# Optimization experiments

Hardware: AMD Instinct MI355X
Metric: run time of the kernel (lower is better)

## Reference

```python
import jax, jax.numpy as jnp
import numpy as np

N_NODES = 20000
N_EDGES = 240000
N_GRAPHS = 200
D_IN = 118
H = 256          # simplified hidden width standing in for the mul=50 irreps hidden
NB = 10          # number_of_basis
RH = 100         # fc_neurons hidden
L = 3            # layers
SH = 9           # lmax=2 -> 1+3+5 spherical-harmonic channels
MAX_RADIUS = 5.0
NUM_NEIGHBORS = 12.0


def setup_inputs() -> dict:
    key = jax.random.key(0)
    ks = jax.random.split(key, 16)
    inp = {
        "x": jax.random.normal(ks[0], (N_NODES, D_IN), jnp.float32),
        "pos": jax.random.normal(ks[1], (N_NODES, 3), jnp.float32),
        "edge_shift": jax.random.normal(ks[2], (N_EDGES, 3), jnp.float32),
        "lattice": jax.random.normal(ks[3], (N_GRAPHS, 3, 3), jnp.float32),
        "W_embed": jax.random.normal(ks[4], (D_IN, H), jnp.float32) / np.sqrt(D_IN),
        "r1": jax.random.normal(ks[5], (L, NB, RH), jnp.float32) / np.sqrt(NB),
        "b1": jax.random.normal(ks[6], (L, RH), jnp.float32) * 0.1,
        "r2": jax.random.normal(ks[7], (L, RH, H), jnp.float32) / np.sqrt(RH),
        "Wtp": jax.random.normal(ks[8], (L, SH, H, H), jnp.float32) / np.sqrt(SH * H),
        "Wself": jax.random.normal(ks[9], (L, H, H), jnp.float32) / np.sqrt(H),
        "Wskip": jax.random.normal(ks[10], (L, H, H), jnp.float32) / np.sqrt(H),
        "Wout": jax.random.normal(ks[11], (H, 1), jnp.float32) / np.sqrt(H),
        "edge_index": jax.random.randint(ks[12], (2, N_EDGES), 0, N_NODES, jnp.int64)
                        if jax.config.jax_enable_x64 else
                      jax.random.randint(ks[12], (2, N_EDGES), 0, N_NODES).astype(jnp.int32),
        "batch": jnp.sort(jax.random.randint(ks[13], (N_NODES,), 0, N_GRAPHS)).astype(jnp.int32),
    }
    return inp


def _sph_harm_lmax2(u):
    """Component-normalized real spherical harmonics up to l=2 on unit vectors u [E,3]."""
    x, y, z = u[:, 0], u[:, 1], u[:, 2]
    c1 = np.sqrt(3.0)
    c2 = np.sqrt(15.0)
    return jnp.stack([
        jnp.ones_like(x),                       # l=0
        c1 * x, c1 * y, c1 * z,                 # l=1
        c2 * x * y, c2 * y * z,                 # l=2
        (np.sqrt(5.0) / 2.0) * (3.0 * z * z - 1.0),
        c2 * x * z, (c2 / 2.0) * (x * x - y * y),
    ], axis=1)                                  # [E, 9]


def _soft_one_hot_cosine(lens):
    """e3nn soft_one_hot_linspace(basis='cosine', cutoff=True) * sqrt(NB)."""
    vals = jnp.linspace(0.0, MAX_RADIUS, NB + 2)
    step = vals[1] - vals[0]
    vals = vals[1:-1]
    diff = (lens[:, None] - vals[None, :]) / step          # [E, NB]
    emb = jnp.cos(0.5 * jnp.pi * diff) * (diff > -1.0) * (diff < 1.0)
    return emb * np.sqrt(float(NB))


def _forward(x, pos, edge_shift, lattice, W_embed, r1, b1, r2, Wtp, Wself, Wskip, Wout,
             edge_src, edge_dst, batch):
    edge_batch = batch[edge_src]                            # [E]
    # periodic edge vectors: pos[dst] - pos[src] + shift @ lattice[graph]
    edge_vec = pos[edge_dst] - pos[edge_src] + jnp.einsum(
        'ni,nij->nj', edge_shift, lattice[edge_batch])      # [E, 3]
    lens = jnp.linalg.norm(edge_vec, axis=1)                # [E]
    u = edge_vec / (lens[:, None] + 1e-12)
    sh = _sph_harm_lmax2(u)                                 # [E, 9]
    emb = _soft_one_hot_cosine(lens)                        # [E, NB]

    h = x @ W_embed                                         # [N, H]
    inv_sqrt_deg = 1.0 / np.sqrt(NUM_NEIGHBORS)
    for l in range(L):
        radial = jax.nn.silu(emb @ r1[l] + b1[l]) @ r2[l]   # [E, H]
        hs = h[edge_src] * radial                           # gather + radial gate
        # weighted tensor-product-like message: sum_a (hs * sh_a) @ Wtp[l, a]
        msg = (hs * sh[:, 0:1]) @ Wtp[l, 0]
        for a in range(1, SH):
            msg = msg + (hs * sh[:, a:a + 1]) @ Wtp[l, a]   # [E, H]
        agg = jax.ops.segment_sum(msg, edge_dst, num_segments=N_NODES) * inv_sqrt_deg
        h = jax.nn.gelu(agg @ Wself[l] + h @ Wskip[l])      # [N, H]

    node_out = h @ Wout                                     # [N, 1]
    # scatter_mean over graphs
    sums = jax.ops.segment_sum(node_out, batch, num_segments=N_GRAPHS)
    cnts = jax.ops.segment_sum(jnp.ones((N_NODES, 1), node_out.dtype), batch,
                               num_segments=N_GRAPHS)
    return sums / jnp.maximum(cnts, 1.0)                    # [G, 1]


def reference(x, pos, edge_shift, lattice, W_embed, r1, b1, r2, Wtp, Wself, Wskip, Wout,
              edge_index, batch):
    return _forward(x, pos, edge_shift, lattice, W_embed, r1, b1, r2, Wtp, Wself, Wskip,
                    Wout, edge_index[0], edge_index[1], batch)
```

## Files before the change

kernel.cpp:

```cpp
#include <hip/hip_runtime.h>
#include <hip/hip_bf16.h>
#include <cstddef>
#include <cstdint>

#define NNODE  20000
#define MPAD   20096
#define NEDGE  240000
#define NGRAPH 200
#define DIN    118
#define HD     256
#define NBASIS 10
#define RHID   100
#define NLAYER 3
#define NSH    9
#define SHSTR  16
#define KTP    (NSH * HD)
#define KTOT   (KTP + HD)
#define KR2    128
#define KEMB   128
#define NRT    (MPAD / 64)

typedef _Float16 f16;
typedef _Float16 f16x2 __attribute__((ext_vector_type(2)));
typedef _Float16 f16x4 __attribute__((ext_vector_type(4)));
typedef _Float16 f16x8 __attribute__((ext_vector_type(8)));
typedef float    f32x4 __attribute__((ext_vector_type(4)));

__device__ __forceinline__ float gelu_tanh(float v) {
  float v3 = v * v * v;
  return 0.5f * v * (1.f + tanhf(0.7978845608028654f * (v + 0.044715f * v3)));
}

__device__ __forceinline__ void gload16(const void* g, void* l) {
  __builtin_amdgcn_global_load_lds(
      (const __attribute__((address_space(1))) unsigned int*)g,
      (__attribute__((address_space(3))) unsigned int*)l, 16, 0, 0);
}

__device__ __forceinline__ int perm64(int rho) {
  return (rho & ~63) | ((rho & 15) * 4 + ((rho >> 4) & 3));
}
__device__ __forceinline__ int inv_perm64(int n) {
  return (n & ~63) | (((n & 3) << 4) | ((n >> 2) & 15));
}

__global__ void deg_hist_kernel(const int* __restrict__ ei, int* __restrict__ deg)
{
  int e = blockIdx.x * 256 + threadIdx.x;
  if (e >= NEDGE) return;
  atomicAdd(&deg[ei[NEDGE + e]], 1);
}

__global__ void scan_kernel(const int* __restrict__ deg, int* __restrict__ rowptr)
{
  __shared__ int part[256];
  int t = threadIdx.x;
  const int chunk = (NNODE + 255) / 256;
  int start = t * chunk;
  int end = min(start + chunk, NNODE);
  int s = 0;
  for (int i = start; i < end; ++i) s += deg[i];
  part[t] = s;
  __syncthreads();
  for (int off = 1; off < 256; off <<= 1) {
    int v = (t >= off) ? part[t - off] : 0;
    __syncthreads();
    part[t] += v;
    __syncthreads();
  }
  int run = (t == 0) ? 0 : part[t - 1];
  for (int i = start; i < end; ++i) { rowptr[i] = run; run += deg[i]; }
  if (t == 255) rowptr[NNODE] = run;
}

__global__ void edge_geom_kernel(const float* __restrict__ pos,
                                 const float* __restrict__ shift,
                                 const float* __restrict__ lat,
                                 const int* __restrict__ ei,
                                 const int* __restrict__ batch,
                                 const int* __restrict__ rowptr,
                                 int* __restrict__ cursor,
                                 f16* __restrict__ sh_s,
                                 float* __restrict__ lens_s)
{
  int e = blockIdx.x * 256 + threadIdx.x;
  if (e >= NEDGE) return;
  int src = ei[e];
  int dst = ei[NEDGE + e];
  int b = batch[src];
  const float* L = lat + (size_t)b * 9;
  float s0 = shift[e * 3 + 0], s1 = shift[e * 3 + 1], s2 = shift[e * 3 + 2];
  float ev[3];
#pragma unroll
  for (int j = 0; j < 3; ++j)
    ev[j] = pos[dst * 3 + j] - pos[src * 3 + j] + s0 * L[j] + s1 * L[3 + j] + s2 * L[6 + j];
  float len = sqrtf(ev[0] * ev[0] + ev[1] * ev[1] + ev[2] * ev[2]);
  float inv = 1.f / (len + 1e-12f);
  float x = ev[0] * inv, y = ev[1] * inv, z = ev[2] * inv;
  const float c1 = 1.7320508075688772f;
  const float c2 = 3.872983346207417f;
  int p = atomicAdd(&cursor[dst], 1);
  int si = rowptr[dst] + p;
  f16* she = sh_s + (size_t)si * SHSTR;
  she[0] = (f16)1.f;
  she[1] = (f16)(c1 * x);
  she[2] = (f16)(c1 * y);
  she[3] = (f16)(c1 * z);
  she[4] = (f16)(c2 * x * y);
  she[5] = (f16)(c2 * y * z);
  she[6] = (f16)(1.1180339887498949f * (3.f * z * z - 1.f));
  she[7] = (f16)(c2 * x * z);
  she[8] = (f16)(1.9364916731037085f * (x * x - y * y));
  she[9] = (f16)0.f;
  *(int*)(she + 10) = src;
  she[12] = (f16)0.f; she[13] = (f16)0.f; she[14] = (f16)0.f; she[15] = (f16)0.f;
  lens_s[si] = len;
}

__global__ void prep_kernel(const float* __restrict__ Wtp_l,
                            const float* __restrict__ Wself_l,
                            const float* __restrict__ Wskip_l,
                            const float* __restrict__ r2l,
                            const float* __restrict__ r1l,
                            const float* __restrict__ b1l,
                            f16* __restrict__ Wtp16,
                            f16* __restrict__ WselfT16,
                            f16* __restrict__ Bcat,
                            f16* __restrict__ r2h,
                            f16* __restrict__ r1h)
{
  int b = blockIdx.x, t = threadIdx.x;
  if (b < KTP) {
    int i = b * 256 + t;
    Wtp16[i] = (f16)Wtp_l[i];
  } else if (b < KTP + 256) {
    int n = b - KTP;
    WselfT16[(size_t)n * HD + t] = (f16)(Wself_l[(size_t)t * HD + n] * 0.28867513459481287f);
  } else if (b < KTP + 512) {
    int rho = b - KTP - 256;
    int pcol = perm64(rho);
    Bcat[(size_t)rho * KTOT + KTP + t] = (f16)Wskip_l[(size_t)t * HD + pcol];
  } else if (b < KTP + 768) {
    int rho = b - KTP - 512;
    if (t < KR2) {
      int p = perm64(rho);
      r2h[(size_t)rho * KR2 + t] = (t < RHID) ? (f16)r2l[(size_t)t * HD + p] : (f16)0.f;
    }
  } else {
#pragma unroll
    for (int u = 0; u < 16; ++u) {
      int idx = u * 256 + t;
      int n = idx >> 5, j = idx & 31;
      float v = 0.f;
      if (n < RHID) {
        if (j < NBASIS) v = r1l[(size_t)j * RHID + n];
        else if (j == NBASIS) v = b1l[n];
      }
      r1h[idx] = (f16)v;
    }
  }
}

__global__ void convert_x_kernel(const float* __restrict__ x, f16* __restrict__ xh)
{
  int i = blockIdx.x * 2 + (threadIdx.x >> 7);
  int k = threadIdx.x & 127;
  xh[(size_t)i * KEMB + k] = (i < NNODE && k < DIN) ? (f16)x[(size_t)i * DIN + k] : (f16)0.f;
}

__global__ void convert_wemb_kernel(const float* __restrict__ Wemb, f16* __restrict__ WembT16)
{
  int n = blockIdx.x, k = threadIdx.x;
  WembT16[(size_t)n * KEMB + k] = (k < DIN) ? (f16)Wemb[(size_t)k * HD + n] : (f16)0.f;
}

__global__ __launch_bounds__(256) void gemm_nt_kernel(
    const f16* __restrict__ A, const f16* __restrict__ B,
    f16* __restrict__ C, int K, int ldc, int permRows)
{
  __shared__ __align__(16) f16 As[4][64][8];
  __shared__ __align__(16) f16 Bs[4][128][8];
  int t = threadIdx.x;
  int lane = t & 63, w = t >> 6;
  int row0 = blockIdx.x * 64;
  int n0 = blockIdx.y * 128;
  f32x4 acc[2][4];
#pragma unroll
  for (int i = 0; i < 2; ++i)
#pragma unroll
    for (int j = 0; j < 4; ++j) acc[i][j] = (f32x4){0.f, 0.f, 0.f, 0.f};
  int mq = (w & 1) * 32, nq = (w >> 1) * 64;
  for (int k0 = 0; k0 < K; k0 += 32) {
    {
      int row = t & 63, cc = t >> 6;
      *(uint4*)&As[cc][row][0] = *(const uint4*)(A + (size_t)(row0 + row) * K + k0 + cc * 8);
    }
#pragma unroll
    for (int u = 0; u < 2; ++u) {
      int idx = t + u * 256;
      int ch = idx >> 7, nn = idx & 127;
      *(uint4*)&Bs[ch][nn][0] = *(const uint4*)(B + (size_t)(n0 + nn) * K + k0 + ch * 8);
    }
    __syncthreads();
    int q = lane >> 4, r = lane & 15;
    f16x8 af[2], bfr[4];
#pragma unroll
    for (int i = 0; i < 2; ++i) af[i] = *(const f16x8*)&As[q][mq + i * 16 + r][0];
#pragma unroll
    for (int j = 0; j < 4; ++j) bfr[j] = *(const f16x8*)&Bs[q][nq + j * 16 + r][0];
#pragma unroll
    for (int i = 0; i < 2; ++i)
#pragma unroll
      for (int j = 0; j < 4; ++j)
        acc[i][j] = __builtin_amdgcn_mfma_f32_16x16x32_f16(af[i], bfr[j], acc[i][j], 0, 0, 0);
    __syncthreads();
  }
  int q4 = ((lane >> 4)) * 4, cl = lane & 15;
#pragma unroll
  for (int i = 0; i < 2; ++i)
#pragma unroll
    for (int rr = 0; rr < 4; ++rr) {
      int row = row0 + mq + i * 16 + q4 + rr;
      int orow = permRows ? inv_perm64(row) : row;
#pragma unroll
      for (int j = 0; j < 4; ++j)
        C[(size_t)orow * ldc + n0 + nq + j * 16 + cl] = (f16)acc[i][j][rr];
    }
}

#define RHSTR 136
__global__ __launch_bounds__(256) void radial_kernel(
    const float* __restrict__ lens_s,
    const f16* __restrict__ r1h,
    const f16* __restrict__ r2h,
    f16* __restrict__ rad)
{
  __shared__ __align__(16) f16 emb_s[64][40];
  __shared__ __align__(16) f16 rhA[64 * RHSTR];
  int t = threadIdx.x;
  int lane = t & 63, w = t >> 6;
  int r = lane & 15, q = lane >> 4;
  int e0 = blockIdx.x * 64;

  {
    float len = lens_s[e0 + lane];
    const float step = 5.f / 11.f;
    const float sq = 3.1622776601683795f;
    f16x8 v;
#pragma unroll
    for (int kk = 0; kk < 8; ++kk) {
      int j = w * 8 + kk;
      float val = 0.f;
      if (j < NBASIS) {
        float d = (len - (float)(j + 1) * step) / step;
        val = (d > -1.f && d < 1.f) ? (__cosf(1.5707963267948966f * d) * sq) : 0.f;
      } else if (j == NBASIS) {
        val = 1.f;
      }
      v[kk] = (f16)val;
    }
    *(f16x8*)&emb_s[lane][w * 8] = v;
  }

  int n0w = w * 64;
  f16x8 bfr[4][4];
#pragma unroll
  for (int j = 0; j < 4; ++j)
#pragma unroll
    for (int ks = 0; ks < 4; ++ks)
      bfr[j][ks] = *(const f16x8*)(r2h + (size_t)(n0w + j * 16 + r) * KR2 + ks * 32 + q * 8);

  f16x8 b1f[2];
#pragma unroll
  for (int j = 0; j < 2; ++j)
    b1f[j] = *(const f16x8*)(r1h + (size_t)((2 * w + j) * 16 + r) * 32 + q * 8);

  __syncthreads();

  f32x4 acc1[4][2];
#pragma unroll
  for (int i = 0; i < 4; ++i)
#pragma unroll
    for (int j = 0; j < 2; ++j) acc1[i][j] = (f32x4){0.f, 0.f, 0.f, 0.f};
  {
    f16x8 a1f[4];
#pragma unroll
    for (int i = 0; i < 4; ++i)
      a1f[i] = *(const f16x8*)&emb_s[i * 16 + r][q * 8];
#pragma unroll
    for (int i = 0; i < 4; ++i)
#pragma unroll
      for (int j = 0; j < 2; ++j)
        acc1[i][j] = __builtin_amdgcn_mfma_f32_16x16x32_f16(a1f[i], b1f[j], acc1[i][j], 0, 0, 0);
  }

#pragma unroll
  for (int i = 0; i < 4; ++i)
#pragma unroll
    for (int j = 0; j < 2; ++j)
#pragma unroll
      for (int rr = 0; rr < 4; ++rr) {
        float s = acc1[i][j][rr];
        s = __fdividef(s, 1.f + __expf(-s));
        rhA[(i * 16 + q * 4 + rr) * RHSTR + (2 * w + j) * 16 + r] = (f16)s;
      }
  __syncthreads();

  f32x4 acc[4][4];
#pragma unroll
  for (int i = 0; i < 4; ++i)
#pragma unroll
    for (int j = 0; j < 4; ++j) acc[i][j] = (f32x4){0.f, 0.f, 0.f, 0.f};
#pragma unroll
  for (int ks = 0; ks < 4; ++ks) {
    f16x8 af[4];
#pragma unroll
    for (int i = 0; i < 4; ++i)
      af[i] = *(const f16x8*)&rhA[(i * 16 + r) * RHSTR + ks * 32 + q * 8];
#pragma unroll
    for (int i = 0; i < 4; ++i)
#pragma unroll
      for (int j = 0; j < 4; ++j)
        acc[i][j] = __builtin_amdgcn_mfma_f32_16x16x32_f16(af[i], bfr[j][ks], acc[i][j], 0, 0, 0);
  }

#pragma unroll
  for (int i = 0; i < 4; ++i)
#pragma unroll
    for (int rr = 0; rr < 4; ++rr) {
      int m = i * 16 + q * 4 + rr;
      f16x4 o;
#pragma unroll
      for (int j = 0; j < 4; ++j) o[j] = (f16)acc[i][j][rr];
      *(f16x4*)(rad + (size_t)(e0 + m) * HD + n0w + r * 4) = o;
    }
}

__global__ __launch_bounds__(256) void gather2_kernel(
    const int* __restrict__ rowptr, const f16* __restrict__ rad,
    const f16* __restrict__ h, const f16* __restrict__ sh_s,
    f16* __restrict__ T)
{
  int t = threadIdx.x;
  int half = t >> 7, lc = t & 127;
  int base = blockIdx.x * 4;
  for (int s = 0; s < 2; ++s) {
    int n = base + s * 2 + half;
    int beg = rowptr[n], end = rowptr[n + 1];
    float a0[NSH], a1[NSH];
#pragma unroll
    for (int a = 0; a < NSH; ++a) { a0[a] = 0.f; a1[a] = 0.f; }
    int j = beg;
    for (; j + 2 <= end; j += 2) {
      const f16* she0 = sh_s + (size_t)j * SHSTR;
      const f16* she1 = she0 + SHSTR;
      f16x8 s80 = *(const f16x8*)she0;
      f16x8 s81 = *(const f16x8*)she1;
      float s8v0 = (float)she0[8];
      float s8v1 = (float)she1[8];
      int src0 = *(const int*)(she0 + 10);
      int src1 = *(const int*)(she1 + 10);
      f16x2 rv0 = *(const f16x2*)(rad + (size_t)j * HD + 2 * lc);
      f16x2 rv1 = *(const f16x2*)(rad + (size_t)(j + 1) * HD + 2 * lc);
      f16x2 hv0 = *(const f16x2*)(h + (size_t)src0 * HD + 2 * lc);
      f16x2 hv1 = *(const f16x2*)(h + (size_t)src1 * HD + 2 * lc);
      float p00 = (float)rv0[0] * (float)hv0[0];
      float p01 = (float)rv0[1] * (float)hv0[1];
      float p10 = (float)rv1[0] * (float)hv1[0];
      float p11 = (float)rv1[1] * (float)hv1[1];
#pragma unroll
      for (int a = 0; a < 8; ++a) {
        float sv0 = (float)s80[a], sv1 = (float)s81[a];
        a0[a] += sv0 * p00 + sv1 * p10;
        a1[a] += sv0 * p01 + sv1 * p11;
      }
      a0[8] += s8v0 * p00 + s8v1 * p10;
      a1[8] += s8v0 * p01 + s8v1 * p11;
    }
    if (j < end) {
      const f16* she = sh_s + (size_t)j * SHSTR;
      f16x8 s8 = *(const f16x8*)she;
      float s8v = (float)she[8];
      int src = *(const int*)(she + 10);
      f16x2 rv = *(const f16x2*)(rad + (size_t)j * HD + 2 * lc);
      f16x2 hv = *(const f16x2*)(h + (size_t)src * HD + 2 * lc);
      float p0 = (float)rv[0] * (float)hv[0];
      float p1 = (float)rv[1] * (float)hv[1];
#pragma unroll
      for (int a = 0; a < 8; ++a) {
        float sv = (float)s8[a];
        a0[a] += sv * p0; a1[a] += sv * p1;
      }
      a0[8] += s8v * p0; a1[8] += s8v * p1;
    }
    f16* Tn = T + (size_t)n * KTP + 2 * lc;
#pragma unroll
    for (int a = 0; a < NSH; ++a) {
      f16x2 o; o[0] = (f16)a0[a]; o[1] = (f16)a1[a];
      *(f16x2*)(Tn + a * HD) = o;
    }
  }
}

#define GBM 64
#define GBN 128
#define NKSTEP (KTOT / 32)
__global__ __launch_bounds__(256) void gemm_fused_kernel(
    const f16* __restrict__ A1,
    const f16* __restrict__ A2,
    const f16* __restrict__ B,
    f16* __restrict__ C)
{
  __shared__ __align__(16) f16 As[2][GBM][4][8];
  __shared__ __align__(16) f16 Bs[2][GBN][4][8];
  int t = threadIdx.x;
  int lane = t & 63, w = t >> 6;
  int row0 = blockIdx.x * GBM;
  int n0 = blockIdx.y * GBN;
  int mq = (w & 1) * 32, nq = (w >> 1) * 64;
  int arow = t >> 2, ach = t & 3;

  f32x4 acc[2][4];
#pragma unroll
  for (int i = 0; i < 2; ++i)
#pragma unroll
    for (int j = 0; j < 4; ++j) acc[i][j] = (f32x4){0.f, 0.f, 0.f, 0.f};

  auto stage = [&](int buf, int k0) {
    const f16* ga = (k0 < KTP)
        ? (A1 + (size_t)(row0 + arow) * KTP + k0 + ach * 8)
        : (A2 + (size_t)(row0 + arow) * HD + (k0 - KTP) + ach * 8);
    gload16(ga, &As[buf][0][0][0] + (size_t)w * 512);
#pragma unroll
    for (int u = 0; u < 2; ++u) {
      int idx = t + u * 256;
      const f16* gb = B + (size_t)(n0 + (idx >> 2)) * KTOT + k0 + (idx & 3) * 8;
      gload16(gb, &Bs[buf][0][0][0] + (size_t)(u * 256 + w * 64) * 8);
    }
  };

  stage(0, 0);
  __syncthreads();

  int cur = 0;
  int q = lane >> 4, r = lane & 15;
  for (int s = 0; s < NKSTEP; ++s) {
    if (s + 1 < NKSTEP) stage(cur ^ 1, (s + 1) * 32);
    f16x8 af[2], bfr[4];
#pragma unroll
    for (int i = 0; i < 2; ++i) af[i] = *(const f16x8*)&As[cur][mq + i * 16 + r][q][0];
#pragma unroll
    for (int j = 0; j < 4; ++j) bfr[j] = *(const f16x8*)&Bs[cur][nq + j * 16 + r][q][0];
#pragma unroll
    for (int i = 0; i < 2; ++i)
#pragma unroll
      for (int j = 0; j < 4; ++j)
        acc[i][j] = __builtin_amdgcn_mfma_f32_16x16x32_f16(af[i], bfr[j], acc[i][j], 0, 0, 0);
    __syncthreads();
    cur ^= 1;
  }

  int q4 = (lane >> 4) * 4, cl = lane & 15;
#pragma unroll
  for (int i = 0; i < 2; ++i)
#pragma unroll
    for (int rr = 0; rr < 4; ++rr) {
      int row = row0 + mq + i * 16 + q4 + rr;
      f16x4 o;
#pragma unroll
      for (int j = 0; j < 4; ++j) o[j] = (f16)gelu_tanh(acc[i][j][rr]);
      *(f16x4*)(C + (size_t)row * HD + n0 + nq + cl * 4) = o;
    }
}

__global__ __launch_bounds__(256) void node_out_fused_kernel(
    const f16* __restrict__ h,
    const float* __restrict__ Wout,
    const int* __restrict__ batch,
    float* __restrict__ out)
{
  __shared__ float red[256];
  int g = blockIdx.x;
  int t = threadIdx.x;
  int lo = 0, hi = NNODE;
  while (lo < hi) { int mid = (lo + hi) >> 1; if (batch[mid] < g) lo = mid + 1; else hi = mid; }
  int start = lo;
  hi = NNODE;
  while (lo < hi) { int mid = (lo + hi) >> 1; if (batch[mid] < g + 1) lo = mid + 1; else hi = mid; }
  int end = lo;
  int half = t >> 7, lc = t & 127;
  float a0 = 0.f, a1 = 0.f;
  for (int n = start + half; n < end; n += 2) {
    f16x2 v = *(const f16x2*)(h + (size_t)n * HD + 2 * lc);
    a0 += (float)v[0];
    a1 += (float)v[1];
  }
  red[t] = a0 * Wout[2 * lc] + a1 * Wout[2 * lc + 1];
  for (int off = 128; off > 0; off >>= 1) {
    __syncthreads();
    if (t < off) red[t] += red[t + off];
  }
  if (t == 0) out[g] = red[0] / fmaxf((float)(end - start), 1.f);
}

extern "C" void kernel_launch(void* const* d_in, const int* in_sizes, int n_in,
                              void* d_out, int out_size, void* d_ws, size_t ws_size,
                              hipStream_t stream)
{
  (void)in_sizes; (void)n_in; (void)out_size;
  const float* x     = (const float*)d_in[0];
  const float* pos   = (const float*)d_in[1];
  const float* shift = (const float*)d_in[2];
  const float* lat   = (const float*)d_in[3];
  const float* Wemb  = (const float*)d_in[4];
  const float* r1    = (const float*)d_in[5];
  const float* b1    = (const float*)d_in[6];
  const float* r2    = (const float*)d_in[7];
  const float* Wtp   = (const float*)d_in[8];
  const float* Wself = (const float*)d_in[9];
  const float* Wskip = (const float*)d_in[10];
  const float* Wout  = (const float*)d_in[11];
  const int*   eidx  = (const int*)d_in[12];
  const int*   batch = (const int*)d_in[13];
  float* out = (float*)d_out;

  char* ws = (char*)d_ws;
  size_t off = 0;
  auto alloc = [&](size_t bytes) -> char* {
    char* p = ws + off;
    off += (bytes + 255) & ~(size_t)255;
    return p;
  };
  f16*   sh_s    = (f16*)alloc((size_t)NEDGE * SHSTR * 2);
  float* lens_s  = (float*)alloc((size_t)NEDGE * 4);
  f16*   hA      = (f16*)alloc((size_t)MPAD * HD * 2);
  f16*   hB      = (f16*)alloc((size_t)MPAD * HD * 2);
  f16*   T       = (f16*)alloc((size_t)MPAD * KTP * 2);
  f16*   rad     = (f16*)alloc((size_t)NEDGE * HD * 2);
  f16*   Bcat    = (f16*)alloc((size_t)HD * KTOT * 2);
  f16*   r2h     = (f16*)alloc((size_t)HD * KR2 * 2);
  f16*   r1hb    = (f16*)alloc((size_t)128 * 32 * 2);
  f16*   Wtp16   = (f16*)alloc((size_t)KTP * HD * 2);
  f16*   WselfT16= (f16*)alloc((size_t)HD * HD * 2);
  int*   rowptr  = (int*)alloc((size_t)(NNODE + 1) * 4);
  int*   deg     = (int*)alloc((size_t)NNODE * 4);
  int*   cursor  = (int*)alloc((size_t)NNODE * 4);
  if (off > ws_size) return;

  f16*   xh      = rad;
  f16*   WembT16 = rad + (size_t)MPAD * KEMB;

  hipMemsetAsync(deg, 0, (size_t)NNODE * 4, stream);
  hipMemsetAsync(cursor, 0, (size_t)NNODE * 4, stream);

  const int EB = (NEDGE + 255) / 256;
  deg_hist_kernel<<<EB, 256, 0, stream>>>(eidx, deg);
  scan_kernel<<<1, 256, 0, stream>>>(deg, rowptr);
  edge_geom_kernel<<<EB, 256, 0, stream>>>(pos, shift, lat, eidx, batch,
                                           rowptr, cursor, sh_s, lens_s);

  convert_x_kernel<<<MPAD / 2, 256, 0, stream>>>(x, xh);
  convert_wemb_kernel<<<HD, KEMB, 0, stream>>>(Wemb, WembT16);
  {
    dim3 eg(MPAD / 64, HD / 128);
    gemm_nt_kernel<<<eg, 256, 0, stream>>>(xh, WembT16, hA, KEMB, HD, 0);
  }

  f16* hcur = hA;
  f16* hnxt = hB;
  dim3 fgrid(NRT, 2);
  dim3 wgrid(HD / 64, KTP / 128);
  for (int l = 0; l < NLAYER; ++l) {
    const float* r1l = r1 + (size_t)l * NBASIS * RHID;
    const float* b1l = b1 + (size_t)l * RHID;
    const float* r2l = r2 + (size_t)l * RHID * HD;
    const float* Wtp_l = Wtp + (size_t)l * NSH * HD * HD;
    const float* Wself_l = Wself + (size_t)l * HD * HD;
    const float* Wskip_l = Wskip + (size_t)l * HD * HD;

    prep_kernel<<<KTP + 768 + 1, 256, 0, stream>>>(Wtp_l, Wself_l, Wskip_l, r2l,
                                                   r1l, b1l,
                                                   Wtp16, WselfT16, Bcat, r2h, r1hb);
    gemm_nt_kernel<<<wgrid, 256, 0, stream>>>(WselfT16, Wtp16, Bcat, HD, KTOT, 1);

    radial_kernel<<<NEDGE / 64, 256, 0, stream>>>(lens_s, r1hb, r2h, rad);
    gather2_kernel<<<NNODE / 4, 256, 0, stream>>>(rowptr, rad, hcur, sh_s, T);
    gemm_fused_kernel<<<fgrid, 256, 0, stream>>>(T, hcur, Bcat, hnxt);
    f16* tmp = hcur; hcur = hnxt; hnxt = tmp;
  }

  node_out_fused_kernel<<<NGRAPH, 256, 0, stream>>>(hcur, Wout, batch, out);
}
```

Before: 721.1 us.

## Deepen GEMM pipeline to four LDS stages and swizzle LDS chunks

The fused GEMM moves from a double-buffered LDS pipeline to a 4-deep ring with three tiles prefetched, using explicit vmcnt waits and a single barrier per k-step instead of two syncthreads. It also XOR-swizzles the 16-byte chunk index on both the global-to-LDS store side and the fragment read side to reduce LDS bank conflicts. This is meant to hide global load latency and cut LDS contention. In exchange it doubles LDS use, which may lower occupancy, and relies on hand-counted vmcnt values matching the three loads issued per stage.

New measurement: 718.4 us. Within noise of the previous version (-0.4%).

```diff
diff --git a/kernel.cpp b/kernel.cpp
--- a/kernel.cpp
+++ b/kernel.cpp
@@ -405,20 +405,24 @@
 #define GBM 64
 #define GBN 128
 #define NKSTEP (KTOT / 32)
+#define NBUF 4
 __global__ __launch_bounds__(256) void gemm_fused_kernel(
     const f16* __restrict__ A1,
     const f16* __restrict__ A2,
     const f16* __restrict__ B,
     f16* __restrict__ C)
 {
-  __shared__ __align__(16) f16 As[2][GBM][4][8];
-  __shared__ __align__(16) f16 Bs[2][GBN][4][8];
+  __shared__ __align__(16) f16 As[NBUF][GBM][4][8];
+  __shared__ __align__(16) f16 Bs[NBUF][GBN][4][8];
   int t = threadIdx.x;
   int lane = t & 63, w = t >> 6;
   int row0 = blockIdx.x * GBM;
   int n0 = blockIdx.y * GBN;
   int mq = (w & 1) * 32, nq = (w >> 1) * 64;
-  int arow = t >> 2, ach = t & 3;
+  int q = lane >> 4, r = lane & 15;
+
+  int arow = t >> 2;
+  int ach = (t & 3) ^ ((t >> 3) & 3);
 
   f32x4 acc[2][4];
 #pragma unroll
@@ -430,34 +434,45 @@
     const f16* ga = (k0 < KTP)
         ? (A1 + (size_t)(row0 + arow) * KTP + k0 + ach * 8)
         : (A2 + (size_t)(row0 + arow) * HD + (k0 - KTP) + ach * 8);
-    gload16(ga, &As[buf][0][0][0] + (size_t)w * 512);
+    gload16(ga, (f16*)As + (size_t)buf * (GBM * 32) + w * 512);
 #pragma unroll
     for (int u = 0; u < 2; ++u) {
       int idx = t + u * 256;
-      const f16* gb = B + (size_t)(n0 + (idx >> 2)) * KTOT + k0 + (idx & 3) * 8;
-      gload16(gb, &Bs[buf][0][0][0] + (size_t)(u * 256 + w * 64) * 8);
+      int brow = idx >> 2;
+      int bch = (idx & 3) ^ ((idx >> 3) & 3);
+      const f16* gb = B + (size_t)(n0 + brow) * KTOT + k0 + bch * 8;
+      gload16(gb, (f16*)Bs + (size_t)buf * (GBN * 32) + (u * 256 + w * 64) * 8);
     }
   };
 
   stage(0, 0);
-  __syncthreads();
-
+  stage(1, 32);
+  stage(2, 64);
+
+  int swz = (q ^ ((r >> 1) & 3)) * 8;
   int cur = 0;
-  int q = lane >> 4, r = lane & 15;
   for (int s = 0; s < NKSTEP; ++s) {
-    if (s + 1 < NKSTEP) stage(cur ^ 1, (s + 1) * 32);
+    if (s <= NKSTEP - 3)      asm volatile("s_waitcnt vmcnt(6)" ::: "memory");
+    else if (s == NKSTEP - 2) asm volatile("s_waitcnt vmcnt(3)" ::: "memory");
+    else                      asm volatile("s_waitcnt vmcnt(0)" ::: "memory");
+    __builtin_amdgcn_s_barrier();
+    if (s + 3 < NKSTEP) stage((cur + 3) & 3, (s + 3) * 32);
+
+    const f16* As_c = (const f16*)As + (size_t)cur * (GBM * 32);
+    const f16* Bs_c = (const f16*)Bs + (size_t)cur * (GBN * 32);
     f16x8 af[2], bfr[4];
 #pragma unroll
-    for (int i = 0; i < 2; ++i) af[i] = *(const f16x8*)&As[cur][mq + i * 16 + r][q][0];
-#pragma unroll
-    for (int j = 0; j < 4; ++j) bfr[j] = *(const f16x8*)&Bs[cur][nq + j * 16 + r][q][0];
+    for (int i = 0; i < 2; ++i)
+      af[i] = *(const f16x8*)(As_c + (mq + i * 16 + r) * 32 + swz);
+#pragma unroll
+    for (int j = 0; j < 4; ++j)
+      bfr[j] = *(const f16x8*)(Bs_c + (nq + j * 16 + r) * 32 + swz);
 #pragma unroll
     for (int i = 0; i < 2; ++i)
 #pragma unroll
       for (int j = 0; j < 4; ++j)
         acc[i][j] = __builtin_amdgcn_mfma_f32_16x16x32_f16(af[i], bfr[j], acc[i][j], 0, 0, 0);
-    __syncthreads();
-    cur ^= 1;
+    cur = (cur + 1) & 3;
   }
 
   int q4 = (lane >> 4) * 4, cl = lane & 15;
```

## Fuse radial MLP with edge gather via node groups of at most 64 edges

Applied to the files above, without the earlier changes.

Adds a single-block kernel that partitions destination-sorted nodes into groups whose edges fit in 64 rows. A new fused kernel computes the radial MLP for each group's edges, multiplies the result by the gathered source features in shared memory, and reduces per node into T. This removes the write and re-read of the large per-edge radial buffer in every layer. In exchange, partially filled 64-edge tiles waste MFMA work, each node's edge reduction runs serially, and any node with more than 64 edges would not fit in a group.

Measured after the change: 764.3 us. 6.0% more time.

```diff
diff --git a/kernel.cpp b/kernel.cpp
--- a/kernel.cpp
+++ b/kernel.cpp
@@ -71,6 +71,47 @@
   int run = (t == 0) ? 0 : part[t - 1];
   for (int i = start; i < end; ++i) { rowptr[i] = run; run += deg[i]; }
   if (t == 255) rowptr[NNODE] = run;
+}
+
+__global__ void group_build_kernel(const int* __restrict__ rowptr,
+                                   int* __restrict__ grp_start,
+                                   int* __restrict__ n_groups)
+{
+  __shared__ int cnts[256];
+  int t = threadIdx.x;
+  const int chunk = (NNODE + 255) / 256;
+  int nbeg = t * chunk;
+  int nend = min(nbeg + chunk, NNODE);
+  int cnt = 0;
+  if (nbeg < nend) {
+    int ebase = rowptr[nbeg];
+    for (int n = nbeg; n < nend; ++n) {
+      if (rowptr[n + 1] - ebase > 64) { ++cnt; ebase = rowptr[n]; }
+    }
+    ++cnt;
+  }
+  cnts[t] = cnt;
+  __syncthreads();
+  for (int off = 1; off < 256; off <<= 1) {
+    int v = (t >= off) ? cnts[t - off] : 0;
+    __syncthreads();
+    cnts[t] += v;
+    __syncthreads();
+  }
+  int g = (t == 0) ? 0 : cnts[t - 1];
+  if (nbeg < nend) {
+    int ebase = rowptr[nbeg];
+    int gstart = nbeg;
+    for (int n = nbeg; n < nend; ++n) {
+      if (rowptr[n + 1] - ebase > 64) {
+        grp_start[g++] = gstart;
+        gstart = n;
+        ebase = rowptr[n];
+      }
+    }
+    grp_start[g++] = gstart;
+  }
+  if (t == 255) { grp_start[cnts[255]] = NNODE; *n_groups = cnts[255]; }
 }
 
 __global__ void edge_geom_kernel(const float* __restrict__ pos,
@@ -229,176 +270,179 @@
 }
 
 #define RHSTR 136
-__global__ __launch_bounds__(256) void radial_kernel(
+#define HSSTR 264
+__global__ __launch_bounds__(256) void radial_gather_kernel(
+    const int* __restrict__ rowptr,
+    const int* __restrict__ grp_start,
+    const int* __restrict__ n_groups,
     const float* __restrict__ lens_s,
+    const f16* __restrict__ sh_s,
+    const f16* __restrict__ h,
     const f16* __restrict__ r1h,
     const f16* __restrict__ r2h,
-    f16* __restrict__ rad)
-{
-  __shared__ __align__(16) f16 emb_s[64][40];
-  __shared__ __align__(16) f16 rhA[64 * RHSTR];
+    f16* __restrict__ T)
+{
+  __shared__ __align__(16) char smem[64 * HSSTR * 2];
+  __shared__ int srcs[64];
+  __shared__ __align__(16) f16 shL[64][16];
+  f16* emb_s = (f16*)smem;
+  f16* rhA   = (f16*)(smem + 64 * 40 * 2);
+  f16* hs_s  = (f16*)smem;
+
   int t = threadIdx.x;
   int lane = t & 63, w = t >> 6;
   int r = lane & 15, q = lane >> 4;
-  int e0 = blockIdx.x * 64;
-
-  {
-    float len = lens_s[e0 + lane];
-    const float step = 5.f / 11.f;
-    const float sq = 3.1622776601683795f;
-    f16x8 v;
-#pragma unroll
-    for (int kk = 0; kk < 8; ++kk) {
-      int j = w * 8 + kk;
-      float val = 0.f;
-      if (j < NBASIS) {
-        float d = (len - (float)(j + 1) * step) / step;
-        val = (d > -1.f && d < 1.f) ? (__cosf(1.5707963267948966f * d) * sq) : 0.f;
-      } else if (j == NBASIS) {
-        val = 1.f;
-      }
-      v[kk] = (f16)val;
-    }
-    *(f16x8*)&emb_s[lane][w * 8] = v;
-  }
-
+  int half = t >> 7, lc = t & 127;
   int n0w = w * 64;
+
   f16x8 bfr[4][4];
 #pragma unroll
   for (int j = 0; j < 4; ++j)
 #pragma unroll
     for (int ks = 0; ks < 4; ++ks)
       bfr[j][ks] = *(const f16x8*)(r2h + (size_t)(n0w + j * 16 + r) * KR2 + ks * 32 + q * 8);
-
   f16x8 b1f[2];
 #pragma unroll
   for (int j = 0; j < 2; ++j)
     b1f[j] = *(const f16x8*)(r1h + (size_t)((2 * w + j) * 16 + r) * 32 + q * 8);
 
-  __syncthreads();
-
-  f32x4 acc1[4][2];
-#pragma unroll
-  for (int i = 0; i < 4; ++i)
-#pragma unroll
-    for (int j = 0; j < 2; ++j) acc1[i][j] = (f32x4){0.f, 0.f, 0.f, 0.f};
-  {
-    f16x8 a1f[4];
+  int ng = *n_groups;
+  for (int g = blockIdx.x; g < ng; g += gridDim.x) {
+    int gn0 = grp_start[g], gn1 = grp_start[g + 1];
+    int ebeg = rowptr[gn0];
+
+    {
+      int e = ebeg + (t >> 2); if (e >= NEDGE) e = NEDGE - 1;
+      *(f16x4*)&shL[t >> 2][(t & 3) * 4] = *(const f16x4*)(sh_s + (size_t)e * SHSTR + (t & 3) * 4);
+    }
+    if (t < 64) {
+      int e = ebeg + t; if (e >= NEDGE) e = NEDGE - 1;
+      srcs[t] = *(const int*)(sh_s + (size_t)e * SHSTR + 10);
+    }
+
+    {
+      int le = ebeg + lane; if (le >= NEDGE) le = NEDGE - 1;
+      float len = lens_s[le];
+      const float step = 5.f / 11.f;
+      const float sq = 3.1622776601683795f;
+      f16x8 v;
+#pragma unroll
+      for (int kk = 0; kk < 8; ++kk) {
+        int j = w * 8 + kk;
+        float val = 0.f;
+        if (j < NBASIS) {
+          float d = (len - (float)(j + 1) * step) / step;
+          val = (d > -1.f && d < 1.f) ? (__cosf(1.5707963267948966f * d) * sq) : 0.f;
+        } else if (j == NBASIS) {
+          val = 1.f;
+        }
+        v[kk] = (f16)val;
+      }
+      *(f16x8*)&emb_s[lane * 40 + w * 8] = v;
+    }
+    __syncthreads();
+
+    f32x4 acc1[4][2];
 #pragma unroll
     for (int i = 0; i < 4; ++i)
-      a1f[i] = *(const f16x8*)&emb_s[i * 16 + r][q * 8];
+#pragma unroll
+      for (int j = 0; j < 2; ++j) acc1[i][j] = (f32x4){0.f, 0.f, 0.f, 0.f};
+    {
+      f16x8 a1f[4];
+#pragma unroll
+      for (int i = 0; i < 4; ++i)
+        a1f[i] = *(const f16x8*)&emb_s[(i * 16 + r) * 40 + q * 8];
+#pragma unroll
+      for (int i = 0; i < 4; ++i)
+#pragma unroll
+        for (int j = 0; j < 2; ++j)
+          acc1[i][j] = __builtin_amdgcn_mfma_f32_16x16x32_f16(a1f[i], b1f[j], acc1[i][j], 0, 0, 0);
+    }
+
 #pragma unroll
     for (int i = 0; i < 4; ++i)
 #pragma unroll
       for (int j = 0; j < 2; ++j)
-        acc1[i][j] = __builtin_amdgcn_mfma_f32_16x16x32_f16(a1f[i], b1f[j], acc1[i][j], 0, 0, 0);
-  }
-
-#pragma unroll
-  for (int i = 0; i < 4; ++i)
-#pragma unroll
-    for (int j = 0; j < 2; ++j)
+#pragma unroll
+        for (int rr = 0; rr < 4; ++rr) {
+          float s = acc1[i][j][rr];
+          s = __fdividef(s, 1.f + __expf(-s));
+          rhA[(i * 16 + q * 4 + rr) * RHSTR + (2 * w + j) * 16 + r] = (f16)s;
+        }
+    __syncthreads();
+
+    f16x4 hv[4][4];
+#pragma unroll
+    for (int i = 0; i < 4; ++i)
 #pragma unroll
       for (int rr = 0; rr < 4; ++rr) {
-        float s = acc1[i][j][rr];
-        s = __fdividef(s, 1.f + __expf(-s));
-        rhA[(i * 16 + q * 4 + rr) * RHSTR + (2 * w + j) * 16 + r] = (f16)s;
+        int m = i * 16 + q * 4 + rr;
+        hv[i][rr] = *(const f16x4*)(h + (size_t)srcs[m] * HD + n0w + r * 4);
       }
-  __syncthreads();
-
-  f32x4 acc[4][4];
-#pragma unroll
-  for (int i = 0; i < 4; ++i)
-#pragma unroll
-    for (int j = 0; j < 4; ++j) acc[i][j] = (f32x4){0.f, 0.f, 0.f, 0.f};
-#pragma unroll
-  for (int ks = 0; ks < 4; ++ks) {
-    f16x8 af[4];
+
+    f32x4 acc[4][4];
 #pragma unroll
     for (int i = 0; i < 4; ++i)
-      af[i] = *(const f16x8*)&rhA[(i * 16 + r) * RHSTR + ks * 32 + q * 8];
+#pragma unroll
+      for (int j = 0; j < 4; ++j) acc[i][j] = (f32x4){0.f, 0.f, 0.f, 0.f};
+#pragma unroll
+    for (int ks = 0; ks < 4; ++ks) {
+      f16x8 af[4];
+#pragma unroll
+      for (int i = 0; i < 4; ++i)
+        af[i] = *(const f16x8*)&rhA[(i * 16 + r) * RHSTR + ks * 32 + q * 8];
+#pragma unroll
+      for (int i = 0; i < 4; ++i)
+#pragma unroll
+        for (int j = 0; j < 4; ++j)
+          acc[i][j] = __builtin_amdgcn_mfma_f32_16x16x32_f16(af[i], bfr[j][ks], acc[i][j], 0, 0, 0);
+    }
+    __syncthreads();
+
 #pragma unroll
     for (int i = 0; i < 4; ++i)
 #pragma unroll
-      for (int j = 0; j < 4; ++j)
-        acc[i][j] = __builtin_amdgcn_mfma_f32_16x16x32_f16(af[i], bfr[j][ks], acc[i][j], 0, 0, 0);
-  }
-
-#pragma unroll
-  for (int i = 0; i < 4; ++i)
-#pragma unroll
-    for (int rr = 0; rr < 4; ++rr) {
-      int m = i * 16 + q * 4 + rr;
-      f16x4 o;
-#pragma unroll
-      for (int j = 0; j < 4; ++j) o[j] = (f16)acc[i][j][rr];
-      *(f16x4*)(rad + (size_t)(e0 + m) * HD + n0w + r * 4) = o;
-    }
-}
-
-__global__ __launch_bounds__(256) void gather2_kernel(
-    const int* __restrict__ rowptr, const f16* __restrict__ rad,
-    const f16* __restrict__ h, const f16* __restrict__ sh_s,
-    f16* __restrict__ T)
-{
-  int t = threadIdx.x;
-  int half = t >> 7, lc = t & 127;
-  int base = blockIdx.x * 4;
-  for (int s = 0; s < 2; ++s) {
-    int n = base + s * 2 + half;
-    int beg = rowptr[n], end = rowptr[n + 1];
-    float a0[NSH], a1[NSH];
-#pragma unroll
-    for (int a = 0; a < NSH; ++a) { a0[a] = 0.f; a1[a] = 0.f; }
-    int j = beg;
-    for (; j + 2 <= end; j += 2) {
-      const f16* she0 = sh_s + (size_t)j * SHSTR;
-      const f16* she1 = she0 + SHSTR;
-      f16x8 s80 = *(const f16x8*)she0;
-      f16x8 s81 = *(const f16x8*)she1;
-      float s8v0 = (float)she0[8];
-      float s8v1 = (float)she1[8];
-      int src0 = *(const int*)(she0 + 10);
-      int src1 = *(const int*)(she1 + 10);
-      f16x2 rv0 = *(const f16x2*)(rad + (size_t)j * HD + 2 * lc);
-      f16x2 rv1 = *(const f16x2*)(rad + (size_t)(j + 1) * HD + 2 * lc);
-      f16x2 hv0 = *(const f16x2*)(h + (size_t)src0 * HD + 2 * lc);
-      f16x2 hv1 = *(const f16x2*)(h + (size_t)src1 * HD + 2 * lc);
-      float p00 = (float)rv0[0] * (float)hv0[0];
-      float p01 = (float)rv0[1] * (float)hv0[1];
-      float p10 = (float)rv1[0] * (float)hv1[0];
-      float p11 = (float)rv1[1] * (float)hv1[1];
-#pragma unroll
-      for (int a = 0; a < 8; ++a) {
-        float sv0 = (float)s80[a], sv1 = (float)s81[a];
-        a0[a] += sv0 * p00 + sv1 * p10;
-        a1[a] += sv0 * p01 + sv1 * p11;
+      for (int rr = 0; rr < 4; ++rr) {
+        int m = i * 16 + q * 4 + rr;
+        f16x4 o;
+#pragma unroll
+        for (int j = 0; j < 4; ++j)
+          o[j] = (f16)(acc[i][j][rr] * (float)hv[i][rr][j]);
+        *(f16x4*)&hs_s[m * HSSTR + n0w + r * 4] = o;
       }
-      a0[8] += s8v0 * p00 + s8v1 * p10;
-      a1[8] += s8v0 * p01 + s8v1 * p11;
-    }
-    if (j < end) {
-      const f16* she = sh_s + (size_t)j * SHSTR;
-      f16x8 s8 = *(const f16x8*)she;
-      float s8v = (float)she[8];
-      int src = *(const int*)(she + 10);
-      f16x2 rv = *(const f16x2*)(rad + (size_t)j * HD + 2 * lc);
-      f16x2 hv = *(const f16x2*)(h + (size_t)src * HD + 2 * lc);
-      float p0 = (float)rv[0] * (float)hv[0];
-      float p1 = (float)rv[1] * (float)hv[1];
-#pragma unroll
-      for (int a = 0; a < 8; ++a) {
-        float sv = (float)s8[a];
-        a0[a] += sv * p0; a1[a] += sv * p1;
+    __syncthreads();
+
+    int npair = (gn1 - gn0 + 1) >> 1;
+    for (int s = 0; s < npair; ++s) {
+      int n = gn0 + s * 2 + half;
+      if (n < gn1) {
+        int beg = rowptr[n] - ebeg, end = rowptr[n + 1] - ebeg;
+        float a0[NSH], a1[NSH];
+#pragma unroll
+        for (int a = 0; a < NSH; ++a) { a0[a] = 0.f; a1[a] = 0.f; }
+        for (int j = beg; j < end; ++j) {
+          f16x2 rv = *(const f16x2*)&hs_s[j * HSSTR + 2 * lc];
+          float p0 = (float)rv[0], p1 = (float)rv[1];
+          f16x8 s8 = *(const f16x8*)&shL[j][0];
+          float s8v = (float)shL[j][8];
+#pragma unroll
+          for (int a = 0; a < 8; ++a) {
+            float sv = (float)s8[a];
+            a0[a] += sv * p0;
+            a1[a] += sv * p1;
+          }
+          a0[8] += s8v * p0;
+          a1[8] += s8v * p1;
+        }
+        f16* Tn = T + (size_t)n * KTP + 2 * lc;
+#pragma unroll
+        for (int a = 0; a < NSH; ++a) {
+          f16x2 o; o[0] = (f16)a0[a]; o[1] = (f16)a1[a];
+          *(f16x2*)(Tn + a * HD) = o;
+        }
       }
-      a0[8] += s8v * p0; a1[8] += s8v * p1;
-    }
-    f16* Tn = T + (size_t)n * KTP + 2 * lc;
-#pragma unroll
-    for (int a = 0; a < NSH; ++a) {
-      f16x2 o; o[0] = (f16)a0[a]; o[1] = (f16)a1[a];
-      *(f16x2*)(Tn + a * HD) = o;
-    }
+    }
+    __syncthreads();
   }
 }
 
@@ -536,7 +580,7 @@
   f16*   hA      = (f16*)alloc((size_t)MPAD * HD * 2);
   f16*   hB      = (f16*)alloc((size_t)MPAD * HD * 2);
   f16*   T       = (f16*)alloc((size_t)MPAD * KTP * 2);
-  f16*   rad     = (f16*)alloc((size_t)NEDGE * HD * 2);
+  f16*   rad     = (f16*)alloc((size_t)MPAD * KEMB * 2 + (size_t)HD * KEMB * 2);
   f16*   Bcat    = (f16*)alloc((size_t)HD * KTOT * 2);
   f16*   r2h     = (f16*)alloc((size_t)HD * KR2 * 2);
   f16*   r1hb    = (f16*)alloc((size_t)128 * 32 * 2);
@@ -545,6 +589,8 @@
   int*   rowptr  = (int*)alloc((size_t)(NNODE + 1) * 4);
   int*   deg     = (int*)alloc((size_t)NNODE * 4);
   int*   cursor  = (int*)alloc((size_t)NNODE * 4);
+  int*   grp     = (int*)alloc((size_t)(NNODE + 2) * 4);
+  int*   ngrp    = (int*)alloc(256);
   if (off > ws_size) return;
 
   f16*   xh      = rad;
@@ -556,6 +602,7 @@
   const int EB = (NEDGE + 255) / 256;
   deg_hist_kernel<<<EB, 256, 0, stream>>>(eidx, deg);
   scan_kernel<<<1, 256, 0, stream>>>(deg, rowptr);
+  group_build_kernel<<<1, 256, 0, stream>>>(rowptr, grp, ngrp);
   edge_geom_kernel<<<EB, 256, 0, stream>>>(pos, shift, lat, eidx, batch,
                                            rowptr, cursor, sh_s, lens_s);
 
@@ -583,8 +630,8 @@
                                                    Wtp16, WselfT16, Bcat, r2h, r1hb);
     gemm_nt_kernel<<<wgrid, 256, 0, stream>>>(WselfT16, Wtp16, Bcat, HD, KTOT, 1);
 
-    radial_kernel<<<NEDGE / 64, 256, 0, stream>>>(lens_s, r1hb, r2h, rad);
-    gather2_kernel<<<NNODE / 4, 256, 0, stream>>>(rowptr, rad, hcur, sh_s, T);
+    radial_gather_kernel<<<4608, 256, 0, stream>>>(rowptr, grp, ngrp, lens_s,
+                                                   sh_s, hcur, r1hb, r2h, T);
     gemm_fused_kernel<<<fgrid, 256, 0, stream>>>(T, hcur, Bcat, hnxt);
     f16* tmp = hcur; hcur = hnxt; hnxt = tmp;
   }
```
